# Kernel optimization log

Measured on AMD Instinct MI355X. Metric: run time of the kernel, lower is better.

Reference implementation:

```python
import jax, jax.numpy as jnp
import numpy as np

NUM_HEADS = 8
NUM_GROUPS = 8
EPS = 1e-5


def setup_inputs() -> dict:
    key = jax.random.key(0)
    ks = jax.random.split(key, 4)
    B, C, H, W = 16, 512, 32, 32
    x = jax.random.normal(ks[0], (B, C, H, W), dtype=jnp.float32)
    gamma = jnp.ones((C,), jnp.float32)
    beta = jnp.zeros((C,), jnp.float32)
    w_qkv = jax.random.normal(ks[1], (3 * C, C), jnp.float32) * (1.0 / np.sqrt(C))
    b_qkv = jnp.zeros((3 * C,), jnp.float32)
    w_out = jax.random.normal(ks[2], (C, C), jnp.float32) * (1.0 / np.sqrt(C))
    b_out = jnp.zeros((C,), jnp.float32)
    return {"x": x, "gamma": gamma, "beta": beta, "w_qkv": w_qkv,
            "b_qkv": b_qkv, "w_out": w_out, "b_out": b_out}


def _group_norm(x, gamma, beta):
    b, c, h, w = x.shape
    xg = x.reshape(b, NUM_GROUPS, c // NUM_GROUPS, h, w)
    mean = xg.mean(axis=(2, 3, 4), keepdims=True)
    var = xg.var(axis=(2, 3, 4), keepdims=True)
    xn = ((xg - mean) * jax.lax.rsqrt(var + EPS)).reshape(b, c, h, w)
    return xn * gamma[None, :, None, None] + beta[None, :, None, None]


def reference(x, gamma, beta, w_qkv, b_qkv, w_out, b_out):
    b, c, h, w = x.shape
    hd = c // NUM_HEADS
    scale = hd ** -0.5
    xn = _group_norm(x, gamma, beta)
    # 1x1 conv == per-pixel linear: (3c, c) x (b, c, h, w) -> (b, 3c, h, w)
    qkv = jnp.einsum('oc,bchw->bohw', w_qkv, xn) + b_qkv[None, :, None, None]
    q, k, v = jnp.split(qkv, 3, axis=1)
    q = q.reshape(b, NUM_HEADS, hd, h * w)
    k = k.reshape(b, NUM_HEADS, hd, h * w)
    v = v.reshape(b, NUM_HEADS, hd, h * w)
    attn = jnp.einsum('bhdi,bhdj->bhij', q, k) * scale  # (b, heads, hw, hw)
    attn = jax.nn.softmax(attn, axis=-1)
    out = jnp.einsum('bhij,bhdj->bhdi', attn, v).reshape(b, c, h, w)
    out = jnp.einsum('oc,bchw->bohw', w_out, out) + b_out[None, :, None, None]
    return x + out
```

## Files before the change

kernel.cpp:

```cpp
#include <hip/hip_runtime.h>
#include <hip/hip_bf16.h>

#define BB   16
#define CCH  512
#define PP   1024
#define NHD  8

typedef unsigned short u16;
typedef unsigned int   u32;
typedef __attribute__((ext_vector_type(8))) short bf16x8;
typedef __attribute__((ext_vector_type(4))) float f32x4;

__device__ __forceinline__ u16 f2bu(float f) {
    __hip_bfloat16 h = __float2bfloat16(f);
    return *reinterpret_cast<u16*>(&h);
}

#define GLOAD_LDS16(gsrc, ldst)                                              \
    __builtin_amdgcn_global_load_lds(                                        \
        (const __attribute__((address_space(1))) u32*)(gsrc),                \
        (__attribute__((address_space(3))) u32*)(ldst), 16, 0, 0)

__launch_bounds__(256)
__global__ void pre_k(const float* __restrict__ x,
                      float* __restrict__ ps, float* __restrict__ pss,
                      const float* __restrict__ w1, const float* __restrict__ w2,
                      u16* __restrict__ d1, u16* __restrict__ d2) {
    int blk = blockIdx.x;
    if (blk < 512) {
        int bg = blk >> 2, part = blk & 3;
        const float4* xp = (const float4*)(x + (size_t)bg * 65536 + (size_t)part * 16384);
        float s = 0.f, ss = 0.f;
        for (int i = threadIdx.x; i < 4096; i += 256) {
            float4 v = xp[i];
            s  += v.x + v.y + v.z + v.w;
            ss += v.x*v.x + v.y*v.y + v.z*v.z + v.w*v.w;
        }
        __shared__ float sh[256], sq[256];
        sh[threadIdx.x] = s; sq[threadIdx.x] = ss;
        __syncthreads();
        for (int off = 128; off > 0; off >>= 1) {
            if (threadIdx.x < off) {
                sh[threadIdx.x] += sh[threadIdx.x + off];
                sq[threadIdx.x] += sq[threadIdx.x + off];
            }
            __syncthreads();
        }
        if (threadIdx.x == 0) {
            ps[blk]  = sh[0];
            pss[blk] = sq[0];
        }
    } else {
        int id = (blk - 512) * 256 + threadIdx.x;
        const float* s; u16* d; int off;
        if (id < 196608) { s = w1; d = d1; off = id * 4; }
        else             { s = w2; d = d2; off = (id - 196608) * 4; }
        float4 v = *(const float4*)(s + off);
        ushort4 o;
        o.x = f2bu(v.x); o.y = f2bu(v.y); o.z = f2bu(v.z); o.w = f2bu(v.w);
        *(ushort4*)(d + off) = o;
    }
}

__launch_bounds__(256)
__global__ void conv_x_k(const float* __restrict__ x,
                         const float* __restrict__ ps, const float* __restrict__ pss,
                         const float* __restrict__ gamma, const float* __restrict__ beta,
                         u16* __restrict__ xbt) {
    __shared__ u16 T[64][73];
    const int tid = threadIdx.x;
    const int p0 = blockIdx.x * 64;
    const int c0 = blockIdx.y * 64;
    const int b  = blockIdx.z;
    const int bg = (b << 3) + (c0 >> 6);
    float s4  = ps[bg*4]  + ps[bg*4+1]  + ps[bg*4+2]  + ps[bg*4+3];
    float ss4 = pss[bg*4] + pss[bg*4+1] + pss[bg*4+2] + pss[bg*4+3];
    float m   = s4 * (1.f / 65536.f);
    float var = ss4 * (1.f / 65536.f) - m * m;
    float rs  = rsqrtf(var + 1e-5f);
    {
        int ci = tid >> 2, psx = (tid & 3) * 16;
        int c = c0 + ci;
        float sc = rs * gamma[c];
        float sf = beta[c] - m * sc;
        const float* xp = x + ((size_t)(b * CCH + c)) * PP + p0 + psx;
        #pragma unroll
        for (int j4 = 0; j4 < 4; j4++) {
            float4 v = *(const float4*)(xp + j4 * 4);
            T[psx + j4*4 + 0][ci] = f2bu(v.x * sc + sf);
            T[psx + j4*4 + 1][ci] = f2bu(v.y * sc + sf);
            T[psx + j4*4 + 2][ci] = f2bu(v.z * sc + sf);
            T[psx + j4*4 + 3][ci] = f2bu(v.w * sc + sf);
        }
    }
    __syncthreads();
    {
        int pi = tid >> 2, cs = (tid & 3) * 16;
        u16* dst = xbt + ((size_t)(b * PP) + p0 + pi) * CCH + c0 + cs;
        #pragma unroll
        for (int j4 = 0; j4 < 4; j4++) {
            ushort4 o;
            o.x = T[pi][cs + j4*4 + 0]; o.y = T[pi][cs + j4*4 + 1];
            o.z = T[pi][cs + j4*4 + 2]; o.w = T[pi][cs + j4*4 + 3];
            *(ushort4*)(dst + j4 * 4) = o;
        }
    }
}

__launch_bounds__(256)
__global__ void mgemm_qkv_k(const u16* __restrict__ Wb, const float* __restrict__ bias,
                            const u16* __restrict__ actT,
                            u16* __restrict__ qT, u16* __restrict__ kT,
                            u16* __restrict__ v) {
    __shared__ __align__(16) u16 smem[17408];
    u16* As = smem;
    u16* Bs = smem + 8192;
    const int tid = threadIdx.x;
    const int id = blockIdx.x;
    const int wk = (id & 7) * 192 + (id >> 3);
    const int b  = wk / 96;
    const int wi = wk % 96;
    const int m0 = (wi >> 3) * 128;
    const int p0 = (wi & 7) * 128;
    const int w = tid >> 6, l = tid & 63, quad = l >> 4, lm = l & 15;
    const int mo = (w >> 1) * 64, no = (w & 1) * 64;

    f32x4 acc[4][4] = {};

    const int srow = (w << 3) + (l >> 3);
    const int scc  = ((l & 7) ^ ((l >> 3) & 7)) << 3;
    const u16* wp = Wb + (size_t)(m0 + srow) * CCH + scc;
    const u16* ap = actT + (size_t)b * PP * CCH + (size_t)(p0 + srow) * CCH + scc;
    const int ldsrow = ((w << 3)) * 64;

    const int c0a = (quad ^ (lm & 7)) << 3;

    for (int k0 = 0; k0 < CCH; k0 += 64) {
        #pragma unroll
        for (int is = 0; is < 4; is++) {
            GLOAD_LDS16(wp + k0 + (size_t)(is * 32) * CCH, &As[is * 2048 + ldsrow]);
            GLOAD_LDS16(ap + k0 + (size_t)(is * 32) * CCH, &Bs[is * 2048 + ldsrow]);
        }
        __syncthreads();
        #pragma unroll
        for (int hf = 0; hf < 2; hf++) {
            const int cofs = hf ? (c0a ^ 32) : c0a;
            bf16x8 af[4], bfr[4];
            #pragma unroll
            for (int mi = 0; mi < 4; mi++)
                af[mi] = *(const bf16x8*)&As[(mo + mi*16 + lm) * 64 + cofs];
            #pragma unroll
            for (int ni = 0; ni < 4; ni++)
                bfr[ni] = *(const bf16x8*)&Bs[(no + ni*16 + lm) * 64 + cofs];
            __builtin_amdgcn_s_setprio(1);
            #pragma unroll
            for (int mi = 0; mi < 4; mi++)
                #pragma unroll
                for (int ni = 0; ni < 4; ni++)
                    acc[mi][ni] = __builtin_amdgcn_mfma_f32_16x16x32_bf16(
                        af[mi], bfr[ni], acc[mi][ni], 0, 0, 0);
            __builtin_amdgcn_s_setprio(0);
        }
        __syncthreads();
    }

    const int region = m0 >> 9;
    if (region < 2) {
        const float scl = (region == 0) ? 0.18033688011f : 1.0f;
        u16* Cb = smem;
        #pragma unroll
        for (int mi = 0; mi < 4; mi++) {
            f32x4 bv = *(const f32x4*)&bias[m0 + mo + mi*16 + quad*4];
            #pragma unroll
            for (int ni = 0; ni < 4; ni++) {
                int colp = no + ni*16 + lm;
                int rowb = mo + mi*16 + quad*4;
                #pragma unroll
                for (int r = 0; r < 4; r++)
                    Cb[colp * 136 + rowb + r] = f2bu((acc[mi][ni][r] + bv[r]) * scl);
            }
        }
        __syncthreads();
        int prow = tid >> 1, half = tid & 1;
        u16* base = (region == 0) ? qT : kT;
        u16* dst = base + ((size_t)b * PP + p0 + prow) * 512 + (m0 & 511) + half * 64;
        const u16* src = &Cb[prow * 136 + half * 64];
        #pragma unroll
        for (int i = 0; i < 8; i++)
            *(uint4*)(dst + i * 8) = *(const uint4*)(src + i * 8);
    } else {
        u16* Cb = smem;
        #pragma unroll
        for (int mi = 0; mi < 4; mi++) {
            f32x4 bv = *(const f32x4*)&bias[m0 + mo + mi*16 + quad*4];
            #pragma unroll
            for (int ni = 0; ni < 4; ni++) {
                int colp = no + ni*16 + lm;
                int rowb = mo + mi*16 + quad*4;
                #pragma unroll
                for (int r = 0; r < 4; r++)
                    Cb[(rowb + r) * 136 + colp] = f2bu(acc[mi][ni][r] + bv[r]);
            }
        }
        __syncthreads();
        int row = tid >> 1, half = tid & 1;
        u16* dst = v + ((size_t)b * 512 + (m0 - 1024) + row) * PP + p0 + half * 64;
        const u16* src = &Cb[row * 136 + half * 64];
        #pragma unroll
        for (int i = 0; i < 8; i++)
            *(uint4*)(dst + i * 8) = *(const uint4*)(src + i * 8);
    }
}

__launch_bounds__(512, 4)
__global__ void fattn_k(const u16* __restrict__ qT, const u16* __restrict__ kT,
                        const u16* __restrict__ v, u16* __restrict__ ao) {
    __shared__ __align__(16) u16 Ps[128 * 136];
    __shared__ __align__(16) u16 Ks[128 * 72];
    __shared__ __align__(16) u16 Vs[64 * 136];
    const int tid = threadIdx.x;
    const int id = blockIdx.x;
    const int wk = ((id & 7) << 7) | (id >> 3);
    const int q0 = (wk & 7) * 128;
    const int pair = wk >> 3;
    const int h = pair & 7;
    const int b = pair >> 3;
    const int w = tid >> 6, l = tid & 63, quad = l >> 4, lm = l & 15;
    const int psw = ((lm >> 2) & 3) << 4;

    {
        int r = w * 16 + (l >> 2), c = (l & 3) * 16;
        int swz = ((l >> 4) & 3) << 4;
        const u16* src = qT + ((size_t)b * PP + q0 + r) * 512 + h * 64 + c;
        *(uint4*)&Ps[r * 136 + (c ^ swz)]     = *(const uint4*)src;
        *(uint4*)&Ps[r * 136 + (c ^ swz) + 8] = *(const uint4*)(src + 8);
    }
    bf16x8 qf0 = *(const bf16x8*)&Ps[(w * 16 + lm) * 136 + ((quad * 8) ^ psw)];
    bf16x8 qf1 = *(const bf16x8*)&Ps[(w * 16 + lm) * 136 + ((32 + quad * 8) ^ psw)];

    bf16x8 onesv;
    #pragma unroll
    for (int i = 0; i < 8; i++) onesv[i] = (short)0x3F80;

    f32x4 O[4] = {};
    f32x4 Ol = {};

    const int ksr = tid >> 2, ksc = (tid & 3) * 16;
    const int vsr = tid >> 3, vsc = (tid & 7) * 16;

    uint4 ka, kb, va, vb;
    {
        const u16* ksrc = kT + ((size_t)b * PP + ksr) * 512 + h * 64 + ksc;
        ka = *(const uint4*)ksrc; kb = *(const uint4*)(ksrc + 8);
        const u16* vsrc = v + ((size_t)b * 512 + h * 64 + vsr) * PP + vsc;
        va = *(const uint4*)vsrc; vb = *(const uint4*)(vsrc + 8);
    }

    for (int j0 = 0; j0 < PP; j0 += 128) {
        __syncthreads();
        *(uint4*)&Ks[ksr * 72 + ksc]      = ka;
        *(uint4*)&Ks[ksr * 72 + ksc + 8]  = kb;
        *(uint4*)&Vs[vsr * 136 + vsc]     = va;
        *(uint4*)&Vs[vsr * 136 + vsc + 8] = vb;
        __syncthreads();

        if (j0 + 128 < PP) {
            const u16* ksrc = kT + ((size_t)b * PP + j0 + 128 + ksr) * 512 + h * 64 + ksc;
            ka = *(const uint4*)ksrc; kb = *(const uint4*)(ksrc + 8);
            const u16* vsrc = v + ((size_t)b * 512 + h * 64 + vsr) * PP + j0 + 128 + vsc;
            va = *(const uint4*)vsrc; vb = *(const uint4*)(vsrc + 8);
        }

        f32x4 s[8];
        __builtin_amdgcn_s_setprio(1);
        #pragma unroll
        for (int ni = 0; ni < 8; ni++) {
            bf16x8 kf0 = *(const bf16x8*)&Ks[(ni*16 + lm) * 72 + quad * 8];
            bf16x8 kf1 = *(const bf16x8*)&Ks[(ni*16 + lm) * 72 + 32 + quad * 8];
            f32x4 z = {};
            z = __builtin_amdgcn_mfma_f32_16x16x32_bf16(qf0, kf0, z, 0, 0, 0);
            s[ni] = __builtin_amdgcn_mfma_f32_16x16x32_bf16(qf1, kf1, z, 0, 0, 0);
        }
        __builtin_amdgcn_s_setprio(0);

        #pragma unroll
        for (int r = 0; r < 4; r++) {
            int rowb = (w * 16 + quad * 4 + r) * 136 + lm;
            #pragma unroll
            for (int ni = 0; ni < 8; ni++) {
                float p = __builtin_amdgcn_exp2f(s[ni][r]);
                Ps[rowb + 16 * (ni ^ quad)] = f2bu(p);
            }
        }

        __builtin_amdgcn_s_setprio(1);
        #pragma unroll
        for (int kf = 0; kf < 4; kf++) {
            bf16x8 pf = *(const bf16x8*)&Ps[(w*16 + lm) * 136 + ((kf * 32 + quad * 8) ^ psw)];
            Ol = __builtin_amdgcn_mfma_f32_16x16x32_bf16(pf, onesv, Ol, 0, 0, 0);
            #pragma unroll
            for (int nd = 0; nd < 4; nd++) {
                bf16x8 vf = *(const bf16x8*)&Vs[(nd*16 + lm) * 136 + kf * 32 + quad * 8];
                O[nd] = __builtin_amdgcn_mfma_f32_16x16x32_bf16(pf, vf, O[nd], 0, 0, 0);
            }
        }
        __builtin_amdgcn_s_setprio(0);
    }

    #pragma unroll
    for (int r = 0; r < 4; r++) {
        float rinv = 1.f / Ol[r];
        int rowb = (w * 16 + quad * 4 + r) * 136 + lm;
        Ps[rowb + 16 * (0 ^ quad)] = f2bu(O[0][r] * rinv);
        Ps[rowb + 16 * (1 ^ quad)] = f2bu(O[1][r] * rinv);
        Ps[rowb + 16 * (2 ^ quad)] = f2bu(O[2][r] * rinv);
        Ps[rowb + 16 * (3 ^ quad)] = f2bu(O[3][r] * rinv);
    }
    {
        int r = w * 16 + (l >> 2), c = (l & 3) * 16;
        int swz = ((l >> 4) & 3) << 4;
        u16* dst = ao + ((size_t)b * PP + q0 + r) * 512 + h * 64 + c;
        *(uint4*)dst       = *(const uint4*)&Ps[r * 136 + (c ^ swz)];
        *(uint4*)(dst + 8) = *(const uint4*)&Ps[r * 136 + (c ^ swz) + 8];
    }
}

__launch_bounds__(256)
__global__ void mgemm_out_k(const u16* __restrict__ Wb, const float* __restrict__ bias,
                            const u16* __restrict__ actT, const float* __restrict__ resid,
                            float* __restrict__ out) {
    __shared__ __align__(16) u16 smem[16384];
    u16* As = smem;
    u16* Bs = smem + 8192;
    const int tid = threadIdx.x;
    const int id = blockIdx.x;
    const int wk = (id & 7) * 64 + (id >> 3);
    const int b  = wk >> 5;
    const int wi = wk & 31;
    const int m0 = (wi >> 3) * 128;
    const int p0 = (wi & 7) * 128;
    const int w = tid >> 6, l = tid & 63, quad = l >> 4, lm = l & 15;
    const int mo = (w >> 1) * 64, no = (w & 1) * 64;

    f32x4 acc[4][4] = {};

    const int srow = (w << 3) + (l >> 3);
    const int scc  = ((l & 7) ^ ((l >> 3) & 7)) << 3;
    const u16* wp = Wb + (size_t)(m0 + srow) * CCH + scc;
    const u16* ap = actT + (size_t)b * PP * CCH + (size_t)(p0 + srow) * CCH + scc;
    const int ldsrow = ((w << 3)) * 64;

    const int c0a = (quad ^ (lm & 7)) << 3;

    for (int k0 = 0; k0 < CCH; k0 += 64) {
        #pragma unroll
        for (int is = 0; is < 4; is++) {
            GLOAD_LDS16(wp + k0 + (size_t)(is * 32) * CCH, &As[is * 2048 + ldsrow]);
            GLOAD_LDS16(ap + k0 + (size_t)(is * 32) * CCH, &Bs[is * 2048 + ldsrow]);
        }
        __syncthreads();
        #pragma unroll
        for (int hf = 0; hf < 2; hf++) {
            const int cofs = hf ? (c0a ^ 32) : c0a;
            bf16x8 af[4], bfr[4];
            #pragma unroll
            for (int mi = 0; mi < 4; mi++)
                af[mi] = *(const bf16x8*)&As[(mo + mi*16 + lm) * 64 + cofs];
            #pragma unroll
            for (int ni = 0; ni < 4; ni++)
                bfr[ni] = *(const bf16x8*)&Bs[(no + ni*16 + lm) * 64 + cofs];
            __builtin_amdgcn_s_setprio(1);
            #pragma unroll
            for (int mi = 0; mi < 4; mi++)
                #pragma unroll
                for (int ni = 0; ni < 4; ni++)
                    acc[mi][ni] = __builtin_amdgcn_mfma_f32_16x16x32_bf16(
                        af[mi], bfr[ni], acc[mi][ni], 0, 0, 0);
            __builtin_amdgcn_s_setprio(0);
        }
        __syncthreads();
    }

    #pragma unroll
    for (int mi = 0; mi < 4; mi++) {
        f32x4 bv = *(const f32x4*)&bias[m0 + mo + mi*16 + quad*4];
        #pragma unroll
        for (int ni = 0; ni < 4; ni++) {
            int p = p0 + no + ni*16 + lm;
            #pragma unroll
            for (int r = 0; r < 4; r++) {
                int m = m0 + mo + mi*16 + quad*4 + r;
                size_t idx = ((size_t)b * CCH + m) * PP + p;
                out[idx] = acc[mi][ni][r] + bv[r] + resid[idx];
            }
        }
    }
}

extern "C" void kernel_launch(void* const* d_in, const int* in_sizes, int n_in,
                              void* d_out, int out_size, void* d_ws, size_t ws_size,
                              hipStream_t stream) {
    const float* x     = (const float*)d_in[0];
    const float* gamma = (const float*)d_in[1];
    const float* beta  = (const float*)d_in[2];
    const float* w_qkv = (const float*)d_in[3];
    const float* b_qkv = (const float*)d_in[4];
    const float* w_out = (const float*)d_in[5];
    const float* b_out = (const float*)d_in[6];

    char* ws = (char*)d_ws;
    float* ps  = (float*)ws;
    float* pss = (float*)(ws + 2048);
    u16* wqb = (u16*)(ws + 4096);
    u16* wob = wqb + 1536 * 512;
    u16* xbt = wob + 512 * 512;
    u16* ao  = xbt + (size_t)BB * PP * CCH;
    u16* qTb = ao  + (size_t)BB * PP * CCH;
    u16* kTb = qTb + (size_t)BB * PP * CCH;
    u16* vb  = kTb + (size_t)BB * PP * CCH;

    pre_k<<<1536, 256, 0, stream>>>(x, ps, pss, w_qkv, w_out, wqb, wob);
    conv_x_k<<<dim3(16, 8, 16), 256, 0, stream>>>(x, ps, pss, gamma, beta, xbt);
    mgemm_qkv_k<<<1536, 256, 0, stream>>>(wqb, b_qkv, xbt, qTb, kTb, vb);
    fattn_k<<<1024, 512, 0, stream>>>(qTb, kTb, vb, ao);
    mgemm_out_k<<<512, 256, 0, stream>>>(wob, b_out, ao, x, (float*)d_out);
}
```

Measured before the change: 231.2 us.

## Enlarge attention query tile to 256 rows with 64-key blocks per iteration

The flash attention kernel now handles 256 query rows per block, with each wave owning two 16-row Q fragments that are loaded straight from global memory into registers. K/V tiles shrink to 64 keys per iteration, and the grid is halved to 512 blocks. Each K/V fragment loaded from shared memory now feeds twice as many MFMAs, cutting LDS and global K/V traffic per unit of work. The costs are higher register pressure, twice as many loop iterations and barriers, and fewer blocks, which may leave CUs underused.

```diff
diff --git a/kernel.cpp b/kernel.cpp
--- a/kernel.cpp
+++ b/kernel.cpp
@@ -215,93 +215,95 @@
 __launch_bounds__(512, 4)
 __global__ void fattn_k(const u16* __restrict__ qT, const u16* __restrict__ kT,
                         const u16* __restrict__ v, u16* __restrict__ ao) {
-    __shared__ __align__(16) u16 Ps[128 * 136];
-    __shared__ __align__(16) u16 Ks[128 * 72];
-    __shared__ __align__(16) u16 Vs[64 * 136];
+    __shared__ __align__(16) u16 Ps[256 * 72];
+    __shared__ __align__(16) u16 Ks[64 * 72];
+    __shared__ __align__(16) u16 Vs[64 * 72];
     const int tid = threadIdx.x;
     const int id = blockIdx.x;
-    const int wk = ((id & 7) << 7) | (id >> 3);
-    const int q0 = (wk & 7) * 128;
-    const int pair = wk >> 3;
+    const int wk = ((id & 7) << 6) | (id >> 3);
+    const int q0 = (wk & 3) * 256;
+    const int pair = wk >> 2;
     const int h = pair & 7;
     const int b = pair >> 3;
     const int w = tid >> 6, l = tid & 63, quad = l >> 4, lm = l & 15;
     const int psw = ((lm >> 2) & 3) << 4;
 
+    bf16x8 qf0a, qf1a, qf0b, qf1b;
     {
-        int r = w * 16 + (l >> 2), c = (l & 3) * 16;
-        int swz = ((l >> 4) & 3) << 4;
-        const u16* src = qT + ((size_t)b * PP + q0 + r) * 512 + h * 64 + c;
-        *(uint4*)&Ps[r * 136 + (c ^ swz)]     = *(const uint4*)src;
-        *(uint4*)&Ps[r * 136 + (c ^ swz) + 8] = *(const uint4*)(src + 8);
-    }
-    bf16x8 qf0 = *(const bf16x8*)&Ps[(w * 16 + lm) * 136 + ((quad * 8) ^ psw)];
-    bf16x8 qf1 = *(const bf16x8*)&Ps[(w * 16 + lm) * 136 + ((32 + quad * 8) ^ psw)];
+        const u16* qsrc = qT + ((size_t)b * PP + q0 + w * 32 + lm) * 512 + h * 64 + quad * 8;
+        qf0a = *(const bf16x8*)qsrc;
+        qf1a = *(const bf16x8*)(qsrc + 32);
+        qf0b = *(const bf16x8*)(qsrc + 16 * 512);
+        qf1b = *(const bf16x8*)(qsrc + 16 * 512 + 32);
+    }
 
     bf16x8 onesv;
     #pragma unroll
     for (int i = 0; i < 8; i++) onesv[i] = (short)0x3F80;
 
-    f32x4 O[4] = {};
-    f32x4 Ol = {};
-
-    const int ksr = tid >> 2, ksc = (tid & 3) * 16;
-    const int vsr = tid >> 3, vsc = (tid & 7) * 16;
-
-    uint4 ka, kb, va, vb;
+    f32x4 Oa[4] = {}, Ob[4] = {};
+    f32x4 Ola = {}, Olb = {};
+
+    const int ksr = tid >> 3, ksc = (tid & 7) * 8;
+
+    uint4 ka, va;
     {
         const u16* ksrc = kT + ((size_t)b * PP + ksr) * 512 + h * 64 + ksc;
-        ka = *(const uint4*)ksrc; kb = *(const uint4*)(ksrc + 8);
-        const u16* vsrc = v + ((size_t)b * 512 + h * 64 + vsr) * PP + vsc;
-        va = *(const uint4*)vsrc; vb = *(const uint4*)(vsrc + 8);
-    }
-
-    for (int j0 = 0; j0 < PP; j0 += 128) {
-        __syncthreads();
-        *(uint4*)&Ks[ksr * 72 + ksc]      = ka;
-        *(uint4*)&Ks[ksr * 72 + ksc + 8]  = kb;
-        *(uint4*)&Vs[vsr * 136 + vsc]     = va;
-        *(uint4*)&Vs[vsr * 136 + vsc + 8] = vb;
-        __syncthreads();
-
-        if (j0 + 128 < PP) {
-            const u16* ksrc = kT + ((size_t)b * PP + j0 + 128 + ksr) * 512 + h * 64 + ksc;
-            ka = *(const uint4*)ksrc; kb = *(const uint4*)(ksrc + 8);
-            const u16* vsrc = v + ((size_t)b * 512 + h * 64 + vsr) * PP + j0 + 128 + vsc;
-            va = *(const uint4*)vsrc; vb = *(const uint4*)(vsrc + 8);
-        }
-
-        f32x4 s[8];
+        ka = *(const uint4*)ksrc;
+        const u16* vsrc = v + ((size_t)b * 512 + h * 64 + ksr) * PP + ksc;
+        va = *(const uint4*)vsrc;
+    }
+
+    for (int j0 = 0; j0 < PP; j0 += 64) {
+        __syncthreads();
+        *(uint4*)&Ks[ksr * 72 + ksc] = ka;
+        *(uint4*)&Vs[ksr * 72 + ksc] = va;
+        __syncthreads();
+
+        if (j0 + 64 < PP) {
+            const u16* ksrc = kT + ((size_t)b * PP + j0 + 64 + ksr) * 512 + h * 64 + ksc;
+            ka = *(const uint4*)ksrc;
+            const u16* vsrc = v + ((size_t)b * 512 + h * 64 + ksr) * PP + j0 + 64 + ksc;
+            va = *(const uint4*)vsrc;
+        }
+
+        f32x4 sa[4], sb[4];
         __builtin_amdgcn_s_setprio(1);
         #pragma unroll
-        for (int ni = 0; ni < 8; ni++) {
+        for (int ni = 0; ni < 4; ni++) {
             bf16x8 kf0 = *(const bf16x8*)&Ks[(ni*16 + lm) * 72 + quad * 8];
             bf16x8 kf1 = *(const bf16x8*)&Ks[(ni*16 + lm) * 72 + 32 + quad * 8];
-            f32x4 z = {};
-            z = __builtin_amdgcn_mfma_f32_16x16x32_bf16(qf0, kf0, z, 0, 0, 0);
-            s[ni] = __builtin_amdgcn_mfma_f32_16x16x32_bf16(qf1, kf1, z, 0, 0, 0);
+            f32x4 za = {}, zb = {};
+            za = __builtin_amdgcn_mfma_f32_16x16x32_bf16(qf0a, kf0, za, 0, 0, 0);
+            sa[ni] = __builtin_amdgcn_mfma_f32_16x16x32_bf16(qf1a, kf1, za, 0, 0, 0);
+            zb = __builtin_amdgcn_mfma_f32_16x16x32_bf16(qf0b, kf0, zb, 0, 0, 0);
+            sb[ni] = __builtin_amdgcn_mfma_f32_16x16x32_bf16(qf1b, kf1, zb, 0, 0, 0);
         }
         __builtin_amdgcn_s_setprio(0);
 
         #pragma unroll
         for (int r = 0; r < 4; r++) {
-            int rowb = (w * 16 + quad * 4 + r) * 136 + lm;
-            #pragma unroll
-            for (int ni = 0; ni < 8; ni++) {
-                float p = __builtin_amdgcn_exp2f(s[ni][r]);
-                Ps[rowb + 16 * (ni ^ quad)] = f2bu(p);
+            int rowa = (w * 32 + quad * 4 + r) * 72 + lm;
+            int rowb_ = (w * 32 + 16 + quad * 4 + r) * 72 + lm;
+            #pragma unroll
+            for (int ni = 0; ni < 4; ni++) {
+                Ps[rowa  + 16 * (ni ^ quad)] = f2bu(__builtin_amdgcn_exp2f(sa[ni][r]));
+                Ps[rowb_ + 16 * (ni ^ quad)] = f2bu(__builtin_amdgcn_exp2f(sb[ni][r]));
             }
         }
 
         __builtin_amdgcn_s_setprio(1);
         #pragma unroll
-        for (int kf = 0; kf < 4; kf++) {
-            bf16x8 pf = *(const bf16x8*)&Ps[(w*16 + lm) * 136 + ((kf * 32 + quad * 8) ^ psw)];
-            Ol = __builtin_amdgcn_mfma_f32_16x16x32_bf16(pf, onesv, Ol, 0, 0, 0);
+        for (int kf = 0; kf < 2; kf++) {
+            bf16x8 pfa = *(const bf16x8*)&Ps[(w*32 + lm) * 72 + ((kf * 32 + quad * 8) ^ psw)];
+            bf16x8 pfb = *(const bf16x8*)&Ps[(w*32 + 16 + lm) * 72 + ((kf * 32 + quad * 8) ^ psw)];
+            Ola = __builtin_amdgcn_mfma_f32_16x16x32_bf16(pfa, onesv, Ola, 0, 0, 0);
+            Olb = __builtin_amdgcn_mfma_f32_16x16x32_bf16(pfb, onesv, Olb, 0, 0, 0);
             #pragma unroll
             for (int nd = 0; nd < 4; nd++) {
-                bf16x8 vf = *(const bf16x8*)&Vs[(nd*16 + lm) * 136 + kf * 32 + quad * 8];
-                O[nd] = __builtin_amdgcn_mfma_f32_16x16x32_bf16(pf, vf, O[nd], 0, 0, 0);
+                bf16x8 vf = *(const bf16x8*)&Vs[(nd*16 + lm) * 72 + kf * 32 + quad * 8];
+                Oa[nd] = __builtin_amdgcn_mfma_f32_16x16x32_bf16(pfa, vf, Oa[nd], 0, 0, 0);
+                Ob[nd] = __builtin_amdgcn_mfma_f32_16x16x32_bf16(pfb, vf, Ob[nd], 0, 0, 0);
             }
         }
         __builtin_amdgcn_s_setprio(0);
@@ -309,19 +311,27 @@
 
     #pragma unroll
     for (int r = 0; r < 4; r++) {
-        float rinv = 1.f / Ol[r];
-        int rowb = (w * 16 + quad * 4 + r) * 136 + lm;
-        Ps[rowb + 16 * (0 ^ quad)] = f2bu(O[0][r] * rinv);
-        Ps[rowb + 16 * (1 ^ quad)] = f2bu(O[1][r] * rinv);
-        Ps[rowb + 16 * (2 ^ quad)] = f2bu(O[2][r] * rinv);
-        Ps[rowb + 16 * (3 ^ quad)] = f2bu(O[3][r] * rinv);
+        float ra = 1.f / Ola[r];
+        float rb = 1.f / Olb[r];
+        int rowa = (w * 32 + quad * 4 + r) * 72 + lm;
+        int rowb_ = (w * 32 + 16 + quad * 4 + r) * 72 + lm;
+        #pragma unroll
+        for (int nd = 0; nd < 4; nd++) {
+            Ps[rowa  + 16 * (nd ^ quad)] = f2bu(Oa[nd][r] * ra);
+            Ps[rowb_ + 16 * (nd ^ quad)] = f2bu(Ob[nd][r] * rb);
+        }
     }
     {
-        int r = w * 16 + (l >> 2), c = (l & 3) * 16;
-        int swz = ((l >> 4) & 3) << 4;
-        u16* dst = ao + ((size_t)b * PP + q0 + r) * 512 + h * 64 + c;
-        *(uint4*)dst       = *(const uint4*)&Ps[r * 136 + (c ^ swz)];
-        *(uint4*)(dst + 8) = *(const uint4*)&Ps[r * 136 + (c ^ swz) + 8];
+        int rr  = w * 32 + (l >> 1);
+        int key = (l >> 3) & 3;
+        int g0  = 2 * (l & 1);
+        u16* dst = ao + ((size_t)b * PP + q0 + rr) * 512 + h * 64 + (l & 1) * 32;
+        const u16* s0 = &Ps[rr * 72 + 16 * (g0 ^ key)];
+        const u16* s1 = &Ps[rr * 72 + 16 * ((g0 + 1) ^ key)];
+        *(uint4*)(dst + 0)  = *(const uint4*)(s0);
+        *(uint4*)(dst + 8)  = *(const uint4*)(s0 + 8);
+        *(uint4*)(dst + 16) = *(const uint4*)(s1);
+        *(uint4*)(dst + 24) = *(const uint4*)(s1 + 8);
     }
 }
 
@@ -422,6 +432,6 @@
     pre_k<<<1536, 256, 0, stream>>>(x, ps, pss, w_qkv, w_out, wqb, wob);
     conv_x_k<<<dim3(16, 8, 16), 256, 0, stream>>>(x, ps, pss, gamma, beta, xbt);
     mgemm_qkv_k<<<1536, 256, 0, stream>>>(wqb, b_qkv, xbt, qTb, kTb, vb);
-    fattn_k<<<1024, 512, 0, stream>>>(qTb, kTb, vb, ao);
+    fattn_k<<<512, 512, 0, stream>>>(qTb, kTb, vb, ao);
     mgemm_out_k<<<512, 256, 0, stream>>>(wob, b_out, ao, x, (float*)d_out);
 }
```

Measured after the change: 217.2 us. -6.0%, faster.
